# Kernel optimization log

Measured on AMD Instinct MI355X. Metric: run time of the kernel, lower is better.

The kernel has to match this reference:

```python
import jax, jax.numpy as jnp
import numpy as np

N = 16384          # nodes
E = 262144         # edges (before self-loops)
FIN_N, FIN_E = 768, 64
F, FE = 256, 128   # node/edge channels
H, C = 8, 32       # heads, per-head dim (H*C == F)
L = 2              # num GATv2 modules
NEG_SLOPE = 0.2


def layer_norm(x, g, b, eps=1e-5):
    mu = jnp.mean(x, axis=-1, keepdims=True)
    var = jnp.mean((x - mu) ** 2, axis=-1, keepdims=True)
    return (x - mu) * jax.lax.rsqrt(var + eps) * g + b


def segment_softmax(logits, seg, n):
    # logits: [Et, H], seg: [Et] destination node ids
    m = jax.ops.segment_max(logits, seg, num_segments=n)
    m = jnp.where(jnp.isfinite(m), m, 0.0)
    e = jnp.exp(logits - m[seg])
    s = jax.ops.segment_sum(e, seg, num_segments=n)
    return e / (s[seg] + 1e-16)


def setup_inputs() -> dict:
    key = jax.random.key(0)
    ks = jax.random.split(key, 20)
    inp = {
        "node_feats": jax.random.normal(ks[0], (N, FIN_N), jnp.float32),
        "edge_index": jax.random.randint(ks[1], (2, E), 0, N, dtype=jnp.int32),
        "edge_attr": jax.random.normal(ks[2], (E, FIN_E), jnp.float32),
        # input projections (bias=False)
        "init_node_w": jax.random.normal(ks[3], (F, FIN_N), jnp.float32) * 0.02,
        "init_edge_w": jax.random.normal(ks[4], (FE, FIN_E), jnp.float32) * 0.02,
        # per-layer GATv2 params, stacked on leading layer dim L
        "lin_l_w": jax.random.normal(ks[5], (L, H * C, F), jnp.float32) * 0.05,
        "lin_l_b": jnp.zeros((L, H * C), jnp.float32),
        "lin_r_w": jax.random.normal(ks[6], (L, H * C, F), jnp.float32) * 0.05,
        "lin_r_b": jnp.zeros((L, H * C), jnp.float32),
        "lin_edge_w": jax.random.normal(ks[7], (L, H * C, FE), jnp.float32) * 0.05,
        "att": jax.random.normal(ks[8], (L, H, C), jnp.float32) * 0.05,
        "gat_bias": jnp.zeros((L, H * C), jnp.float32),
        # block params
        "ln1_g": jnp.ones((L, F), jnp.float32), "ln1_b": jnp.zeros((L, F), jnp.float32),
        "mlp_w1": jax.random.normal(ks[9], (L, 2 * F, F), jnp.float32) * 0.05,
        "mlp_w2": jax.random.normal(ks[10], (L, F, 2 * F), jnp.float32) * 0.05,
        "ln2_g": jnp.ones((L, F), jnp.float32), "ln2_b": jnp.zeros((L, F), jnp.float32),
    }
    return inp


def _gatv2_module(x, src, dst, e_emb, p, l, n):
    # e_emb: [Et, H, C] already projected edge embeddings (incl. self-loops)
    x_l = (x @ p["lin_l_w"][l].T + p["lin_l_b"][l]).reshape(n, H, C)
    x_r = (x @ p["lin_r_w"][l].T + p["lin_r_b"][l]).reshape(n, H, C)
    m = x_l[src] + x_r[dst] + e_emb                    # [Et, H, C]
    g = jnp.where(m >= 0, m, NEG_SLOPE * m)            # leaky_relu(0.2)
    logits = jnp.einsum('ehc,hc->eh', g, p["att"][l])
    alpha = segment_softmax(logits, dst, n)            # [Et, H]
    out = jax.ops.segment_sum(alpha[:, :, None] * x_l[src], dst, num_segments=n)
    out = out.reshape(n, H * C) + p["gat_bias"][l]
    # residual -> LN -> MLP -> residual -> LN  (dropout=0, eval mode)
    h = layer_norm(x + out, p["ln1_g"][l], p["ln1_b"][l])
    y = jax.nn.gelu(h @ p["mlp_w1"][l].T, approximate=False) @ p["mlp_w2"][l].T
    return layer_norm(h + y, p["ln2_g"][l], p["ln2_b"][l])


def reference(node_feats, edge_index, edge_attr, init_node_w, init_edge_w,
              lin_l_w, lin_l_b, lin_r_w, lin_r_b, lin_edge_w, att, gat_bias,
              ln1_g, ln1_b, mlp_w1, mlp_w2, ln2_g, ln2_b):
    p = dict(lin_l_w=lin_l_w, lin_l_b=lin_l_b, lin_r_w=lin_r_w, lin_r_b=lin_r_b,
             lin_edge_w=lin_edge_w, att=att, gat_bias=gat_bias, ln1_g=ln1_g,
             ln1_b=ln1_b, mlp_w1=mlp_w1, mlp_w2=mlp_w2, ln2_g=ln2_g, ln2_b=ln2_b)
    x = node_feats @ init_node_w.T                     # [N, F]
    ea = edge_attr @ init_edge_w.T                     # [E, FE]
    src, dst = edge_index[0], edge_index[1]
    # add self loops with fill_value='mean' (mean of incoming edge_attr per node)
    cnt = jax.ops.segment_sum(jnp.ones((E,), ea.dtype), dst, num_segments=N)
    loop_attr = jax.ops.segment_sum(ea, dst, num_segments=N) / jnp.maximum(cnt, 1.0)[:, None]
    ea_all = jnp.concatenate([ea, loop_attr], axis=0)  # [E+N, FE]
    ar = jnp.arange(N, dtype=src.dtype)
    src_all = jnp.concatenate([src, ar])
    dst_all = jnp.concatenate([dst, ar])
    for l in range(L):
        e_emb = (ea_all @ lin_edge_w[l].T).reshape(-1, H, C)
        x = _gatv2_module(x, src_all, dst_all, e_emb, p, l, N)
    return x
```

## Files before the change

### kernel.cpp

```cpp
#include <hip/hip_runtime.h>

typedef unsigned short u16;
typedef __attribute__((ext_vector_type(8))) short s8v;
typedef __attribute__((ext_vector_type(4))) float f4v;

#define NN 16384
#define EE 262144
#define ET (EE + NN)
#define NTILES (ET / 64)

__device__ __forceinline__ float bfu(u16 h){ return __uint_as_float((unsigned)h << 16); }
__device__ __forceinline__ u16 f2bf(float f){
  unsigned u = __float_as_uint(f);
  unsigned r = u + 0x7FFFu + ((u >> 16) & 1u);
  return (u16)(r >> 16);
}
__device__ __forceinline__ float ldf(const void* p, size_t i, int isbf){
  return isbf ? bfu(((const u16*)p)[i]) : ((const float*)p)[i];
}
__device__ __forceinline__ float gelu_f(float x){ return 0.5f*x*(1.0f+erff(x*0.7071067811865475f)); }

__device__ __forceinline__ uint4 load8bf(const void* p, size_t eoff, int isbf){
  if (isbf) return *(const uint4*)((const u16*)p + eoff);
  const float* f = (const float*)p + eoff;
  uint4 r;
  r.x = (unsigned)f2bf(f[0]) | ((unsigned)f2bf(f[1])<<16);
  r.y = (unsigned)f2bf(f[2]) | ((unsigned)f2bf(f[3])<<16);
  r.z = (unsigned)f2bf(f[4]) | ((unsigned)f2bf(f[5])<<16);
  r.w = (unsigned)f2bf(f[6]) | ((unsigned)f2bf(f[7])<<16);
  return r;
}

__device__ __forceinline__ void gload16(const void* g, void* l){
  __builtin_amdgcn_global_load_lds((const __attribute__((address_space(1))) void*)g,
                                   (__attribute__((address_space(3))) void*)l, 16, 0, 0);
}

__global__ void k_detect(const void* nf, int* flag)
{
  int t = threadIdx.x;
  const float* f = (const float*)nf;
  int cnt = 0;
  for (int i = t; i < 4096; i += 256) {
    float a = fabsf(f[i]);
    if (a > 1e-5f && a < 100.0f) cnt++;
  }
  __shared__ int s[256];
  s[t] = cnt; __syncthreads();
  for (int st = 128; st > 0; st >>= 1) { if (t < st) s[t] += s[t+st]; __syncthreads(); }
  if (t == 0) *flag = (s[0] < 2048) ? 1 : 0;
}

__global__ void k_cvt(const void* __restrict__ in, u16* __restrict__ out, const int* __restrict__ dflag)
{
  int isbf = *dflag;
  size_t i = ((size_t)blockIdx.x*256 + threadIdx.x)*8;
  *(uint4*)&out[i] = load8bf(in, i, isbf);
}

__global__ void k_wcvt(const void* __restrict__ lw, const void* __restrict__ rw,
                       const void* __restrict__ w1, const void* __restrict__ w2,
                       const void* __restrict__ iw, u16* __restrict__ wall,
                       const int* __restrict__ dflag)
{
  int isbf = *dflag;
  size_t i = ((size_t)blockIdx.x*256 + threadIdx.x)*8;
  const void* src; size_t off;
  if (i < 196608) { src = iw; off = i; }
  else {
    size_t j = i - 196608;
    size_t l = j / 393216; j -= l*393216;
    if (j < 65536)       { src = lw; off = l*65536 + j; }
    else if (j < 131072) { src = rw; off = l*65536 + (j - 65536); }
    else if (j < 262144) { src = w1; off = l*131072 + (j - 131072); }
    else                 { src = w2; off = l*131072 + (j - 262144); }
  }
  *(uint4*)&wall[i] = load8bf(src, off, isbf);
}

template<int KK, int NJ, int ACT, int CFMT>
__global__ __launch_bounds__(256)
void mg4(const u16* __restrict__ A, const u16* __restrict__ B,
         const void* __restrict__ bias1, const void* __restrict__ bias2,
         size_t bioff, int nsplit, int has_bias,
         void* __restrict__ C, void* __restrict__ C2, int N,
         const int* __restrict__ dflag)
{
  __shared__ u16 As[32][512];
  int isbf = *dflag;
  int t = threadIdx.x;
  int w = t>>6, lane = t&63, l4 = lane&15, quad = lane>>4;

  int nwg = gridDim.x*gridDim.y;
  int wg  = blockIdx.y*gridDim.x + blockIdx.x;
  int lg  = (wg & 7)*(nwg >> 3) + (wg >> 3);
  int bx  = lg % gridDim.x, by = lg / gridDim.x;
  int bm = by*64, bn = bx*(64*NJ);

  const u16* gA = A + (size_t)(bm + w*16 + l4)*KK + quad*8;
  const u16* gB[NJ];
  #pragma unroll
  for (int j=0;j<NJ;++j)
    gB[j] = B + (size_t)(bn + (NJ*w + j)*16 + l4)*KK + quad*8;

  f4v acc[4][NJ];
  f4v zero = {0.f,0.f,0.f,0.f};
  #pragma unroll
  for (int i=0;i<4;++i)
    #pragma unroll
    for (int j=0;j<NJ;++j) acc[i][j] = zero;

  #pragma unroll
  for (int kc=0; kc<KK/256; ++kc) {
    if (kc) __syncthreads();
    s8v breg[8][NJ];
    #pragma unroll
    for (int c=0;c<8;++c)
      #pragma unroll
      for (int j=0;j<NJ;++j)
        breg[c][j] = *(const s8v*)(gB[j] + kc*256 + c*32);
    #pragma unroll
    for (int c=0;c<8;++c)
      gload16(gA + kc*256 + c*32, &As[c*4 + w][0]);
    __syncthreads();
    #pragma unroll
    for (int c=0;c<8;++c) {
      s8v a[4];
      #pragma unroll
      for (int i=0;i<4;++i) a[i] = *(const s8v*)&As[c*4 + i][lane*8];
      #pragma unroll
      for (int i=0;i<4;++i)
        #pragma unroll
        for (int j=0;j<NJ;++j)
          acc[i][j] = __builtin_amdgcn_mfma_f32_16x16x32_bf16(a[i], breg[c][j], acc[i][j], 0,0,0);
    }
  }

  #pragma unroll
  for (int i=0;i<4;++i)
    #pragma unroll
    for (int j=0;j<NJ;++j) {
      int cj = bn + (NJ*w + j)*16 + l4;
      float bvs = 0.f;
      if (has_bias) bvs = (cj < nsplit) ? ldf(bias1, bioff + cj, isbf)
                                        : ldf(bias2, bioff + cj - nsplit, isbf);
      #pragma unroll
      for (int r=0;r<4;++r) {
        int row = bm + i*16 + quad*4 + r;
        float v = acc[i][j][r] + bvs;
        if (ACT==1) v = gelu_f(v);
        if (CFMT==1) ((u16*)C)[(size_t)row*N + cj] = f2bf(v);
        else {
          ((float*)C)[(size_t)row*N + cj] = v;
          if (CFMT==2) ((u16*)C2)[(size_t)row*N + cj] = f2bf(v);
        }
      }
    }
}

__global__ void k_count(const int* __restrict__ dst, int* __restrict__ deg)
{
  int e = blockIdx.x*256 + threadIdx.x;
  if (e >= ET) return;
  int d = (e < EE) ? dst[e] : (e - EE);
  atomicAdd(&deg[d], 1);
}

__global__ void k_scan(const int* __restrict__ deg, int* __restrict__ rowstart)
{
  __shared__ int csum[256];
  int t = threadIdx.x;
  int s = 0;
  for (int i=0;i<64;i++) s += deg[t*64+i];
  csum[t] = s;
  __syncthreads();
  if (t == 0) {
    int r = 0;
    for (int i=0;i<256;i++){ int v = csum[i]; csum[i] = r; r += v; }
    rowstart[NN] = r;
  }
  __syncthreads();
  int b = csum[t];
  for (int i=0;i<64;i++){ rowstart[t*64+i] = b; b += deg[t*64+i]; }
}

__global__ void k_scatter(const int* __restrict__ src, const int* __restrict__ dst,
                          const int* __restrict__ rowstart,
                          int* __restrict__ fill, int* __restrict__ csr,
                          int* __restrict__ srcc, int* __restrict__ dstc)
{
  int e = blockIdx.x*256 + threadIdx.x;
  if (e >= ET) return;
  int d  = (e < EE) ? dst[e] : (e - EE);
  int sv = (e < EE) ? src[e] : (e - EE);
  int pos = rowstart[d] + atomicAdd(&fill[d], 1);
  csr[pos]  = e;
  srcc[pos] = sv;
  dstc[pos] = d;
}

__global__ __launch_bounds__(256)
void k_lm_acsr(const int* __restrict__ csr, const int* __restrict__ rowstart,
               const void* __restrict__ edge_attr, u16* __restrict__ attr_csr,
               const int* __restrict__ dflag)
{
  int isbf = *dflag;
  int j = threadIdx.x & 63, wid = threadIdx.x >> 6;
  int n = blockIdx.x*4 + wid;
  int s = rowstart[n], e1 = rowstart[n+1];
  float sum = 0.f; int cnt = 0; int selfpos = s;
  for (int p = s; p < e1; ++p) {
    int eid = csr[p];
    if (eid < EE) {
      float v = ldf(edge_attr, (size_t)eid*64 + j, isbf);
      attr_csr[(size_t)p*64 + j] = f2bf(v);
      sum += v; cnt++;
    } else selfpos = p;
  }
  attr_csr[(size_t)selfpos*64 + j] = f2bf(sum / (float)max(cnt, 1));
}

__global__ void k_wc(const void* __restrict__ We, const void* __restrict__ iew,
                     u16* __restrict__ Wcb, const int* __restrict__ dflag)
{
  int isbf = *dflag;
  int idx = blockIdx.x*256 + threadIdx.x;
  int j = idx & 63, c = (idx >> 6) & 255, l = idx >> 14;
  float s = 0.f;
  for (int k=0;k<128;k++) s += ldf(We, ((size_t)l*256 + c)*128 + k, isbf) * ldf(iew, (size_t)k*64 + j, isbf);
  Wcb[idx] = f2bf(s);
}

__global__ __launch_bounds__(256)
void k_elogits(const int* __restrict__ srcc, const int* __restrict__ dstc,
               const u16* __restrict__ Wcb, const u16* __restrict__ xlr,
               const u16* __restrict__ attr_csr,
               const void* __restrict__ att, size_t att_off,
               float* __restrict__ logits, const int* __restrict__ dflag)
{
  int isbf = *dflag;
  __shared__ u16 WcF[32*64*8];
  __shared__ float satt[256];

  int t = threadIdx.x;
  int w = t>>6, lane = t&63, l4 = lane&15, quad = lane>>4;

  satt[t] = ldf(att, att_off + t, isbf);
  #pragma unroll
  for (int f = 0; f < 8; ++f) {
    int fr = w + f*4;
    int i = fr >> 1, ks = fr & 1;
    *(uint4*)&WcF[(fr*64 + lane)*8] = *(const uint4*)&Wcb[(size_t)(16*i + l4)*64 + ks*32 + quad*8];
  }
  __syncthreads();

  f4v zero = {0.f,0.f,0.f,0.f};
  int me = w*16 + l4;
  for (int tile = blockIdx.x; tile < NTILES; tile += gridDim.x) {
    int epos = tile*64 + me;
    int sn = srcc[epos], dn = dstc[epos];
    s8v b0 = *(const s8v*)&attr_csr[(size_t)epos*64 + quad*8];
    s8v b1 = *(const s8v*)&attr_csr[(size_t)epos*64 + 32 + quad*8];

    f4v acc[16];
    #pragma unroll
    for (int i=0;i<16;++i){
      s8v a0 = *(const s8v*)&WcF[((2*i  )*64 + lane)*8];
      s8v a1 = *(const s8v*)&WcF[((2*i+1)*64 + lane)*8];
      acc[i] = __builtin_amdgcn_mfma_f32_16x16x32_bf16(a0, b0, zero, 0,0,0);
      acc[i] = __builtin_amdgcn_mfma_f32_16x16x32_bf16(a1, b1, acc[i], 0,0,0);
    }

    float ph[8] = {0.f,0.f,0.f,0.f,0.f,0.f,0.f,0.f};
    #pragma unroll
    for (int i=0;i<16;++i){
      uint2 xlv = *(const uint2*)&xlr[(size_t)sn*512 +       i*16 + quad*4];
      uint2 xrv = *(const uint2*)&xlr[(size_t)dn*512 + 256 + i*16 + quad*4];
      float4 av = *(const float4*)&satt[i*16 + quad*4];
      float m0 = acc[i][0] + bfu((u16)(xlv.x & 0xffff)) + bfu((u16)(xrv.x & 0xffff));
      float m1 = acc[i][1] + bfu((u16)(xlv.x >> 16))    + bfu((u16)(xrv.x >> 16));
      float m2 = acc[i][2] + bfu((u16)(xlv.y & 0xffff)) + bfu((u16)(xrv.y & 0xffff));
      float m3 = acc[i][3] + bfu((u16)(xlv.y >> 16))    + bfu((u16)(xrv.y >> 16));
      float g0 = fmaxf(m0, 0.2f*m0), g1 = fmaxf(m1, 0.2f*m1);
      float g2 = fmaxf(m2, 0.2f*m2), g3 = fmaxf(m3, 0.2f*m3);
      ph[i>>1] += av.x*g0 + av.y*g1 + av.z*g2 + av.w*g3;
    }
    #pragma unroll
    for (int h=0;h<8;++h){
      ph[h] += __shfl_xor(ph[h], 16);
      ph[h] += __shfl_xor(ph[h], 32);
    }
    if (quad == 0){
      float4 lo = {ph[0], ph[1], ph[2], ph[3]};
      float4 hi = {ph[4], ph[5], ph[6], ph[7]};
      *(float4*)&logits[(size_t)epos*8]     = lo;
      *(float4*)&logits[(size_t)epos*8 + 4] = hi;
    }
  }
}

__global__ __launch_bounds__(256)
void k_aggln(const int* __restrict__ srcc, const int* __restrict__ rowstart,
             const float* __restrict__ logits, const u16* __restrict__ xlr, const float* __restrict__ xbuf,
             const void* __restrict__ gat_bias, const void* __restrict__ ln1g, const void* __restrict__ ln1b,
             size_t poff, float* __restrict__ hbuf, u16* __restrict__ hbufb, const int* __restrict__ dflag)
{
  int isbf = *dflag;
  int lane = threadIdx.x & 63, wid = threadIdx.x >> 6;
  int n = blockIdx.x*4 + wid;
  int s = rowstart[n], deg = rowstart[n+1] - s;
  int myh = lane >> 3;
  float mrun = -3.0e38f, lrun = 0.f;
  float a0=0.f, a1=0.f, a2=0.f, a3=0.f;

  for (int c0 = 0; c0 < deg; c0 += 64) {
    int idx = s + c0 + lane; if (idx >= ET) idx = ET-1;
    int sv = srcc[idx];
    int lim = min(64, deg - c0);
    size_t lbase = (size_t)(s + c0)*8 + myh;
    for (int j = 0; j < lim; ++j) {
      int sn  = __shfl(sv, j);
      float lg = logits[lbase + (size_t)j*8];
      uint2 xv = *(const uint2*)&xlr[(size_t)sn*512 + 4*lane];
      float mn = fmaxf(mrun, lg);
      float sc = __expf(mrun - mn);
      float wv = __expf(lg - mn);
      mrun = mn;
      lrun = lrun*sc + wv;
      a0 = a0*sc + wv*bfu((u16)(xv.x & 0xffff));
      a1 = a1*sc + wv*bfu((u16)(xv.x >> 16));
      a2 = a2*sc + wv*bfu((u16)(xv.y & 0xffff));
      a3 = a3*sc + wv*bfu((u16)(xv.y >> 16));
    }
  }
  float inv = 1.f/(lrun + 1e-16f);
  int c = 4*lane;
  float4 res = *(const float4*)&xbuf[(size_t)n*256 + c];
  float o0 = a0*inv + ldf(gat_bias, poff+c+0, isbf) + res.x;
  float o1 = a1*inv + ldf(gat_bias, poff+c+1, isbf) + res.y;
  float o2 = a2*inv + ldf(gat_bias, poff+c+2, isbf) + res.z;
  float o3 = a3*inv + ldf(gat_bias, poff+c+3, isbf) + res.w;

  float v = o0+o1+o2+o3;
  #pragma unroll
  for (int off=1; off<64; off<<=1) v += __shfl_xor(v, off);
  float mu = v * (1.f/256.f);
  float d0=o0-mu, d1=o1-mu, d2=o2-mu, d3=o3-mu;
  float v2 = d0*d0+d1*d1+d2*d2+d3*d3;
  #pragma unroll
  for (int off=1; off<64; off<<=1) v2 += __shfl_xor(v2, off);
  float wn = rsqrtf(v2*(1.f/256.f) + 1e-5f);
  float4 outv;
  outv.x = d0*wn*ldf(ln1g, poff+c+0, isbf) + ldf(ln1b, poff+c+0, isbf);
  outv.y = d1*wn*ldf(ln1g, poff+c+1, isbf) + ldf(ln1b, poff+c+1, isbf);
  outv.z = d2*wn*ldf(ln1g, poff+c+2, isbf) + ldf(ln1b, poff+c+2, isbf);
  outv.w = d3*wn*ldf(ln1g, poff+c+3, isbf) + ldf(ln1b, poff+c+3, isbf);
  *(float4*)&hbuf[(size_t)n*256 + c] = outv;
  uint2 hb;
  hb.x = (unsigned)f2bf(outv.x) | ((unsigned)f2bf(outv.y)<<16);
  hb.y = (unsigned)f2bf(outv.z) | ((unsigned)f2bf(outv.w)<<16);
  *(uint2*)&hbufb[(size_t)n*256 + c] = hb;
}

__global__ __launch_bounds__(256)
void k_ln_add(const float* __restrict__ a, const u16* __restrict__ b2,
              const void* __restrict__ gg, const void* __restrict__ bb, size_t poff,
              float* __restrict__ out, u16* __restrict__ outb, const int* __restrict__ dflag)
{
  int isbf = *dflag;
  int n = blockIdx.x, t = threadIdx.x;
  __shared__ float r[256];
  float x = a[(size_t)n*256 + t] + bfu(b2[(size_t)n*256 + t]);
  r[t] = x; __syncthreads();
  for (int st = 128; st > 0; st >>= 1) { if (t < st) r[t] += r[t+st]; __syncthreads(); }
  float mu = r[0] * (1.f/256.f);
  __syncthreads();
  float d = x - mu;
  r[t] = d*d; __syncthreads();
  for (int st = 128; st > 0; st >>= 1) { if (t < st) r[t] += r[t+st]; __syncthreads(); }
  float var = r[0] * (1.f/256.f);
  float o = d * rsqrtf(var + 1e-5f) * ldf(gg, poff + t, isbf) + ldf(bb, poff + t, isbf);
  out[(size_t)n*256 + t] = o;
  outb[(size_t)n*256 + t] = f2bf(o);
}

__global__ void k_out(const float* __restrict__ x, void* __restrict__ out, const int* __restrict__ dflag)
{
  int isbf = *dflag;
  int i = blockIdx.x*256 + threadIdx.x;
  if (isbf) ((u16*)out)[i] = f2bf(x[i]);
  else      ((float*)out)[i] = x[i];
}

extern "C" void kernel_launch(void* const* d_in, const int* in_sizes, int n_in,
                              void* d_out, int out_size, void* d_ws, size_t ws_size,
                              hipStream_t stream)
{
  const void* node_feats = d_in[0];
  const int*  edge_index = (const int*)d_in[1];
  const void* edge_attr  = d_in[2];
  const void* init_node_w= d_in[3];
  const void* init_edge_w= d_in[4];
  const void* lin_l_w    = d_in[5];
  const void* lin_l_b    = d_in[6];
  const void* lin_r_w    = d_in[7];
  const void* lin_r_b    = d_in[8];
  const void* lin_edge_w = d_in[9];
  const void* att        = d_in[10];
  const void* gat_bias   = d_in[11];
  const void* ln1_g      = d_in[12];
  const void* ln1_b      = d_in[13];
  const void* mlp_w1     = d_in[14];
  const void* mlp_w2     = d_in[15];
  const void* ln2_g      = d_in[16];
  const void* ln2_b      = d_in[17];

  const int* srcp = edge_index;
  const int* dstp = edge_index + EE;

  char* p = (char*)d_ws;
  auto alloc = [&](size_t bytes) { void* r = (void*)p; p += (bytes + 255) & ~(size_t)255; return r; };
  int*   dflag   = (int*)alloc(256);
  int*   deg     = (int*)alloc((size_t)NN*4);
  int*   rowstart= (int*)alloc((size_t)(NN+1)*4);
  int*   fill    = (int*)alloc((size_t)NN*4);
  int*   csr     = (int*)alloc((size_t)ET*4);
  int*   srcc    = (int*)alloc((size_t)ET*4);
  int*   dstc    = (int*)alloc((size_t)ET*4);
  u16*   Wcb     = (u16*)alloc((size_t)2*256*64*2);
  u16*   wall    = (u16*)alloc((size_t)983040*2);
  u16*   attr_csr= (u16*)alloc((size_t)ET*64*2);
  float* logits  = (float*)alloc((size_t)ET*8*4);
  float* hbuf    = (float*)alloc((size_t)NN*256*4);
  float* xbuf    = (float*)alloc((size_t)NN*256*4);
  u16*   xbufb   = (u16*)alloc((size_t)NN*256*2);
  u16*   hbufb   = (u16*)alloc((size_t)NN*256*2);
  u16*   xlr     = (u16*)alloc((size_t)NN*512*2);
  u16*   nfb     = (u16*)logits;
  u16*   ymid    = xlr;
  u16*   y2      = (u16*)d_out;

  u16* Wn = wall;

  hipMemsetAsync(deg,  0, (size_t)NN*4, stream);
  hipMemsetAsync(fill, 0, (size_t)NN*4, stream);

  k_detect <<<1, 256, 0, stream>>>(node_feats, dflag);

  k_count  <<<(ET+255)/256, 256, 0, stream>>>(dstp, deg);
  k_scan   <<<1, 256, 0, stream>>>(deg, rowstart);
  k_scatter<<<(ET+255)/256, 256, 0, stream>>>(srcp, dstp, rowstart, fill, csr, srcc, dstc);
  k_lm_acsr<<<NN/4, 256, 0, stream>>>(csr, rowstart, edge_attr, attr_csr, dflag);

  k_wc     <<<128, 256, 0, stream>>>(lin_edge_w, init_edge_w, Wcb, dflag);
  k_wcvt   <<<480, 256, 0, stream>>>(lin_l_w, lin_r_w, mlp_w1, mlp_w2, init_node_w, wall, dflag);

  k_cvt<<<(NN*768)/(8*256), 256, 0, stream>>>(node_feats, nfb, dflag);
  mg4<768,1,0,2><<<dim3(4, NN/64), 256, 0, stream>>>(nfb, Wn, nullptr, nullptr, 0, 1<<29, 0,
                                                     xbuf, xbufb, 256, dflag);

  for (int l = 0; l < 2; ++l) {
    size_t bo = (size_t)l*256;
    u16* Wlr = wall + 196608 + (size_t)l*393216;
    u16* W1  = Wlr + 131072;
    u16* W2  = Wlr + 262144;
    mg4<256,2,0,1><<<dim3(4, NN/64), 256, 0, stream>>>(xbufb, Wlr, lin_l_b, lin_r_b, bo, 256, 1,
                                                       xlr, nullptr, 512, dflag);
    k_elogits<<<1024, 256, 0, stream>>>(srcc, dstc, Wcb + (size_t)l*256*64, xlr,
                                        attr_csr, att, (size_t)l*256, logits, dflag);
    k_aggln<<<NN/4, 256, 0, stream>>>(srcc, rowstart, logits, xlr, xbuf,
                                      gat_bias, ln1_g, ln1_b, bo, hbuf, hbufb, dflag);
    mg4<256,2,1,1><<<dim3(4, NN/64), 256, 0, stream>>>(hbufb, W1, nullptr, nullptr, 0, 1<<29, 0,
                                                       ymid, nullptr, 512, dflag);
    mg4<512,1,0,1><<<dim3(4, NN/64), 256, 0, stream>>>(ymid, W2, nullptr, nullptr, 0, 1<<29, 0,
                                                       y2, nullptr, 256, dflag);
    k_ln_add<<<NN, 256, 0, stream>>>(hbuf, y2, ln2_g, ln2_b, bo, xbuf, xbufb, dflag);
  }

  k_out<<<(NN*256)/256, 256, 0, stream>>>(xbuf, d_out, dflag);
}
```

Baseline: 714.3 us.

## Permute xlr column layout so edge-logit kernel gathers 16-byte vectors

The lin_l/lin_r GEMM now writes its bf16 output with a column permutation, so each MFMA lane's features for two consecutive 16-column tiles are contiguous. The edge-logit kernel then loads one uint4 per source and destination node instead of many uint2 gathers, and processes tile pairs together to shorten accumulator lifetimes. The aggregation kernel's gather index is remapped to match the permuted layout. k_elogits also gets an occupancy hint in its launch bounds. This risks layout mismatches between producer and consumers, and lower-width scattered stores in the GEMM epilogue.

```diff
diff --git a/kernel.cpp b/kernel.cpp
--- a/kernel.cpp
+++ b/kernel.cpp
@@ -34,6 +34,10 @@
 __device__ __forceinline__ void gload16(const void* g, void* l){
   __builtin_amdgcn_global_load_lds((const __attribute__((address_space(1))) void*)g,
                                    (__attribute__((address_space(3))) void*)l, 16, 0, 0);
+}
+
+__device__ __forceinline__ int permc(int c){
+  return ((c>>2)&3)*64 + ((c&255)>>4)*4 + (c&3);
 }
 
 __global__ void k_detect(const void* nf, int* flag)
@@ -78,7 +82,7 @@
   *(uint4*)&wall[i] = load8bf(src, off, isbf);
 }
 
-template<int KK, int NJ, int ACT, int CFMT>
+template<int KK, int NJ, int ACT, int CFMT, int PERM>
 __global__ __launch_bounds__(256)
 void mg4(const u16* __restrict__ A, const u16* __restrict__ B,
          const void* __restrict__ bias1, const void* __restrict__ bias2,
@@ -144,12 +148,13 @@
       float bvs = 0.f;
       if (has_bias) bvs = (cj < nsplit) ? ldf(bias1, bioff + cj, isbf)
                                         : ldf(bias2, bioff + cj - nsplit, isbf);
+      int cjs = PERM ? ((cj & ~255) | permc(cj)) : cj;
       #pragma unroll
       for (int r=0;r<4;++r) {
         int row = bm + i*16 + quad*4 + r;
         float v = acc[i][j][r] + bvs;
         if (ACT==1) v = gelu_f(v);
-        if (CFMT==1) ((u16*)C)[(size_t)row*N + cj] = f2bf(v);
+        if (CFMT==1) ((u16*)C)[(size_t)row*N + cjs] = f2bf(v);
         else {
           ((float*)C)[(size_t)row*N + cj] = v;
           if (CFMT==2) ((u16*)C2)[(size_t)row*N + cj] = f2bf(v);
@@ -231,7 +236,7 @@
   Wcb[idx] = f2bf(s);
 }
 
-__global__ __launch_bounds__(256)
+__global__ __launch_bounds__(256, 4)
 void k_elogits(const int* __restrict__ srcc, const int* __restrict__ dstc,
                const u16* __restrict__ Wcb, const u16* __restrict__ xlr,
                const u16* __restrict__ attr_csr,
@@ -262,28 +267,39 @@
     s8v b0 = *(const s8v*)&attr_csr[(size_t)epos*64 + quad*8];
     s8v b1 = *(const s8v*)&attr_csr[(size_t)epos*64 + 32 + quad*8];
 
-    f4v acc[16];
-    #pragma unroll
-    for (int i=0;i<16;++i){
-      s8v a0 = *(const s8v*)&WcF[((2*i  )*64 + lane)*8];
-      s8v a1 = *(const s8v*)&WcF[((2*i+1)*64 + lane)*8];
-      acc[i] = __builtin_amdgcn_mfma_f32_16x16x32_bf16(a0, b0, zero, 0,0,0);
-      acc[i] = __builtin_amdgcn_mfma_f32_16x16x32_bf16(a1, b1, acc[i], 0,0,0);
-    }
-
-    float ph[8] = {0.f,0.f,0.f,0.f,0.f,0.f,0.f,0.f};
-    #pragma unroll
-    for (int i=0;i<16;++i){
-      uint2 xlv = *(const uint2*)&xlr[(size_t)sn*512 +       i*16 + quad*4];
-      uint2 xrv = *(const uint2*)&xlr[(size_t)dn*512 + 256 + i*16 + quad*4];
-      float4 av = *(const float4*)&satt[i*16 + quad*4];
-      float m0 = acc[i][0] + bfu((u16)(xlv.x & 0xffff)) + bfu((u16)(xrv.x & 0xffff));
-      float m1 = acc[i][1] + bfu((u16)(xlv.x >> 16))    + bfu((u16)(xrv.x >> 16));
-      float m2 = acc[i][2] + bfu((u16)(xlv.y & 0xffff)) + bfu((u16)(xrv.y & 0xffff));
-      float m3 = acc[i][3] + bfu((u16)(xlv.y >> 16))    + bfu((u16)(xrv.y >> 16));
+    float ph[8];
+    #pragma unroll
+    for (int h=0;h<8;++h) ph[h] = 0.f;
+
+    #pragma unroll
+    for (int ip=0; ip<8; ++ip){
+      int i0 = 2*ip, i1 = 2*ip+1;
+      s8v a00 = *(const s8v*)&WcF[((2*i0  )*64 + lane)*8];
+      s8v a01 = *(const s8v*)&WcF[((2*i0+1)*64 + lane)*8];
+      s8v a10 = *(const s8v*)&WcF[((2*i1  )*64 + lane)*8];
+      s8v a11 = *(const s8v*)&WcF[((2*i1+1)*64 + lane)*8];
+      f4v acc0 = __builtin_amdgcn_mfma_f32_16x16x32_bf16(a00, b0, zero, 0,0,0);
+      acc0     = __builtin_amdgcn_mfma_f32_16x16x32_bf16(a01, b1, acc0, 0,0,0);
+      f4v acc1 = __builtin_amdgcn_mfma_f32_16x16x32_bf16(a10, b0, zero, 0,0,0);
+      acc1     = __builtin_amdgcn_mfma_f32_16x16x32_bf16(a11, b1, acc1, 0,0,0);
+      uint4 xlv = *(const uint4*)&xlr[(size_t)sn*512 +       quad*64 + ip*8];
+      uint4 xrv = *(const uint4*)&xlr[(size_t)dn*512 + 256 + quad*64 + ip*8];
+      float4 av0 = *(const float4*)&satt[i0*16 + quad*4];
+      float4 av1 = *(const float4*)&satt[i1*16 + quad*4];
+      float m0 = acc0[0] + bfu((u16)(xlv.x & 0xffff)) + bfu((u16)(xrv.x & 0xffff));
+      float m1 = acc0[1] + bfu((u16)(xlv.x >> 16))    + bfu((u16)(xrv.x >> 16));
+      float m2 = acc0[2] + bfu((u16)(xlv.y & 0xffff)) + bfu((u16)(xrv.y & 0xffff));
+      float m3 = acc0[3] + bfu((u16)(xlv.y >> 16))    + bfu((u16)(xrv.y >> 16));
       float g0 = fmaxf(m0, 0.2f*m0), g1 = fmaxf(m1, 0.2f*m1);
       float g2 = fmaxf(m2, 0.2f*m2), g3 = fmaxf(m3, 0.2f*m3);
-      ph[i>>1] += av.x*g0 + av.y*g1 + av.z*g2 + av.w*g3;
+      float s0 = av0.x*g0 + av0.y*g1 + av0.z*g2 + av0.w*g3;
+      m0 = acc1[0] + bfu((u16)(xlv.z & 0xffff)) + bfu((u16)(xrv.z & 0xffff));
+      m1 = acc1[1] + bfu((u16)(xlv.z >> 16))    + bfu((u16)(xrv.z >> 16));
+      m2 = acc1[2] + bfu((u16)(xlv.w & 0xffff)) + bfu((u16)(xrv.w & 0xffff));
+      m3 = acc1[3] + bfu((u16)(xlv.w >> 16))    + bfu((u16)(xrv.w >> 16));
+      g0 = fmaxf(m0, 0.2f*m0); g1 = fmaxf(m1, 0.2f*m1);
+      g2 = fmaxf(m2, 0.2f*m2); g3 = fmaxf(m3, 0.2f*m3);
+      ph[ip] = s0 + av1.x*g0 + av1.y*g1 + av1.z*g2 + av1.w*g3;
     }
     #pragma unroll
     for (int h=0;h<8;++h){
@@ -310,6 +326,7 @@
   int n = blockIdx.x*4 + wid;
   int s = rowstart[n], deg = rowstart[n+1] - s;
   int myh = lane >> 3;
+  int pxl = ((lane&3)<<6) + ((lane>>2)<<2);
   float mrun = -3.0e38f, lrun = 0.f;
   float a0=0.f, a1=0.f, a2=0.f, a3=0.f;
 
@@ -321,7 +338,7 @@
     for (int j = 0; j < lim; ++j) {
       int sn  = __shfl(sv, j);
       float lg = logits[lbase + (size_t)j*8];
-      uint2 xv = *(const uint2*)&xlr[(size_t)sn*512 + 4*lane];
+      uint2 xv = *(const uint2*)&xlr[(size_t)sn*512 + pxl];
       float mn = fmaxf(mrun, lg);
       float sc = __expf(mrun - mn);
       float wv = __expf(lg - mn);
@@ -456,24 +473,24 @@
   k_wcvt   <<<480, 256, 0, stream>>>(lin_l_w, lin_r_w, mlp_w1, mlp_w2, init_node_w, wall, dflag);
 
   k_cvt<<<(NN*768)/(8*256), 256, 0, stream>>>(node_feats, nfb, dflag);
-  mg4<768,1,0,2><<<dim3(4, NN/64), 256, 0, stream>>>(nfb, Wn, nullptr, nullptr, 0, 1<<29, 0,
-                                                     xbuf, xbufb, 256, dflag);
+  mg4<768,1,0,2,0><<<dim3(4, NN/64), 256, 0, stream>>>(nfb, Wn, nullptr, nullptr, 0, 1<<29, 0,
+                                                       xbuf, xbufb, 256, dflag);
 
   for (int l = 0; l < 2; ++l) {
     size_t bo = (size_t)l*256;
     u16* Wlr = wall + 196608 + (size_t)l*393216;
     u16* W1  = Wlr + 131072;
     u16* W2  = Wlr + 262144;
-    mg4<256,2,0,1><<<dim3(4, NN/64), 256, 0, stream>>>(xbufb, Wlr, lin_l_b, lin_r_b, bo, 256, 1,
-                                                       xlr, nullptr, 512, dflag);
+    mg4<256,2,0,1,1><<<dim3(4, NN/64), 256, 0, stream>>>(xbufb, Wlr, lin_l_b, lin_r_b, bo, 256, 1,
+                                                         xlr, nullptr, 512, dflag);
     k_elogits<<<1024, 256, 0, stream>>>(srcc, dstc, Wcb + (size_t)l*256*64, xlr,
                                         attr_csr, att, (size_t)l*256, logits, dflag);
     k_aggln<<<NN/4, 256, 0, stream>>>(srcc, rowstart, logits, xlr, xbuf,
                                       gat_bias, ln1_g, ln1_b, bo, hbuf, hbufb, dflag);
-    mg4<256,2,1,1><<<dim3(4, NN/64), 256, 0, stream>>>(hbufb, W1, nullptr, nullptr, 0, 1<<29, 0,
-                                                       ymid, nullptr, 512, dflag);
-    mg4<512,1,0,1><<<dim3(4, NN/64), 256, 0, stream>>>(ymid, W2, nullptr, nullptr, 0, 1<<29, 0,
-                                                       y2, nullptr, 256, dflag);
+    mg4<256,2,1,1,0><<<dim3(4, NN/64), 256, 0, stream>>>(hbufb, W1, nullptr, nullptr, 0, 1<<29, 0,
+                                                         ymid, nullptr, 512, dflag);
+    mg4<512,1,0,1,0><<<dim3(4, NN/64), 256, 0, stream>>>(ymid, W2, nullptr, nullptr, 0, 1<<29, 0,
+                                                         y2, nullptr, 256, dflag);
     k_ln_add<<<NN, 256, 0, stream>>>(hbuf, y2, ln2_g, ln2_b, bo, xbuf, xbufb, dflag);
   }
 
```

Result: slower. 966.4 us (+35.3%).
